# Optimization experiments

Hardware: AMD Instinct MI355X
Metric: run time of the kernel (lower is better)

Reference implementation:

```python
import jax, jax.numpy as jnp
import numpy as np

K = 3  # polynomial filter order

def gfgcn_layer(X, S, W, h, b):
    # X: [N, in], W: [in, out], h: [K], b: [out]
    X = X @ W
    X_out = h[0] * X
    Sx = X
    for k in range(1, K):
        Sx = S @ Sx                 # graph shift propagation
        X_out = X_out + h[k] * Sx   # scalar-weighted accumulate
    return X_out + b[None, :]


def setup_inputs() -> dict:
    key = jax.random.key(0)
    ks = jax.random.split(key, 12)
    N, in_dim, hid_dim, out_dim = 8192, 512, 128, 64
    # scale S so repeated propagation stays numerically tame
    S = jax.random.normal(ks[0], (N, N), dtype=jnp.float32) / jnp.sqrt(jnp.float32(N))
    X = jax.random.normal(ks[1], (N, in_dim), dtype=jnp.float32)
    def kaiming(k, shape):
        bound = np.sqrt(6.0 / shape[0])
        return jax.random.uniform(k, shape, jnp.float32, -bound, bound)
    W1 = kaiming(ks[2], (in_dim, hid_dim))
    W2 = kaiming(ks[3], (hid_dim, hid_dim))
    W3 = kaiming(ks[4], (hid_dim, out_dim))
    h1 = jnp.ones((K,), jnp.float32)
    h2 = jnp.ones((K,), jnp.float32)
    h3 = jnp.ones((K,), jnp.float32)
    b1 = jnp.zeros((hid_dim,), jnp.float32)
    b2 = jnp.zeros((hid_dim,), jnp.float32)
    b3 = jnp.zeros((out_dim,), jnp.float32)
    return {"S": S, "X": X, "W1": W1, "h1": h1, "b1": b1,
            "W2": W2, "h2": h2, "b2": b2, "W3": W3, "h3": h3, "b3": b3}


def reference(S, X, W1, h1, b1, W2, h2, b2, W3, h3, b3):
    # layer 1 + ReLU (dropout p=0 -> identity, batch_norm=False)
    X = jax.nn.relu(gfgcn_layer(X, S, W1, h1, b1))
    # layer 2 + ReLU
    X = jax.nn.relu(gfgcn_layer(X, S, W2, h2, b2))
    # last layer, last_act = Identity
    return gfgcn_layer(X, S, W3, h3, b3)
```

## Files before the change

### kernel.cpp

```cpp
#include <hip/hip_runtime.h>


typedef __attribute__((ext_vector_type(4))) float  f32x4;
typedef __attribute__((ext_vector_type(8))) __bf16 bf16x8;
typedef __attribute__((ext_vector_type(4))) __bf16 bf16x4;

__device__ __forceinline__ void gload_lds16(const __bf16* g, __bf16* l) {
    __builtin_amdgcn_global_load_lds(
        (const __attribute__((address_space(1))) void*)g,
        (__attribute__((address_space(3))) void*)l, 16, 0, 0);
}

__global__ void cvt_f32_bf16(const float4* __restrict__ in,
                             bf16x4* __restrict__ out, int n4) {
    int i  = blockIdx.x * blockDim.x + threadIdx.x;
    int st = gridDim.x * blockDim.x;
    for (; i < n4; i += st) {
        float4 v = in[i];
        bf16x4 o;
        o[0] = (__bf16)v.x; o[1] = (__bf16)v.y;
        o[2] = (__bf16)v.z; o[3] = (__bf16)v.w;
        out[i] = o;
    }
}

__global__ void cvt_transpose(const float* __restrict__ W,
                              __bf16* __restrict__ Wt, int Kd, int Md) {
    int i = blockIdx.x * blockDim.x + threadIdx.x;
    if (i < Kd * Md) {
        int k = i / Md, m = i % Md;
        Wt[(size_t)m * Kd + k] = (__bf16)W[i];
    }
}

template<int MF, int NF, int OUTMODE, int BF32>
__global__ __launch_bounds__(256)
void gemm_rd(const __bf16* __restrict__ A, const void* __restrict__ Bv,
             void* __restrict__ out, int K, int Kchunk, int Mtot, int Ntot)
{
    const int lane = threadIdx.x & 63;
    const int w    = threadIdx.x >> 6;
    const int l15  = lane & 15;
    const int quad = lane >> 4;

    const int m_base = blockIdx.x * (64 * MF) + w * (16 * MF);
    const int n_base = blockIdx.y * (16 * NF);
    const int kstart = blockIdx.z * Kchunk;

    const __bf16* Ap[MF];
    #pragma unroll
    for (int mf = 0; mf < MF; mf++)
        Ap[mf] = A + (size_t)(m_base + mf * 16 + l15) * K + kstart + quad * 8;

    const __bf16* Bp[NF];
    const float*  Bpf[NF];
    #pragma unroll
    for (int nf = 0; nf < NF; nf++) {
        const size_t roff = (size_t)(n_base + nf * 16 + l15) * K + kstart + quad * 8;
        if (BF32) Bpf[nf] = (const float*)Bv + roff;
        else      Bp[nf]  = (const __bf16*)Bv + roff;
    }

    f32x4 acc[MF][NF];
    #pragma unroll
    for (int mf = 0; mf < MF; mf++)
        #pragma unroll
        for (int nf = 0; nf < NF; nf++)
            acc[mf][nf] = (f32x4){0.f, 0.f, 0.f, 0.f};

    #pragma unroll 2
    for (int ks = 0; ks < Kchunk; ks += 32) {
        bf16x8 a[MF], b[NF];
        #pragma unroll
        for (int mf = 0; mf < MF; mf++) a[mf] = *(const bf16x8*)(Ap[mf] + ks);
        #pragma unroll
        for (int nf = 0; nf < NF; nf++) {
            if (BF32) {
                float4 f0 = *(const float4*)(Bpf[nf] + ks);
                float4 f1 = *(const float4*)(Bpf[nf] + ks + 4);
                bf16x8 tt;
                tt[0] = (__bf16)f0.x; tt[1] = (__bf16)f0.y;
                tt[2] = (__bf16)f0.z; tt[3] = (__bf16)f0.w;
                tt[4] = (__bf16)f1.x; tt[5] = (__bf16)f1.y;
                tt[6] = (__bf16)f1.z; tt[7] = (__bf16)f1.w;
                b[nf] = tt;
            } else {
                b[nf] = *(const bf16x8*)(Bp[nf] + ks);
            }
        }
        #pragma unroll
        for (int mf = 0; mf < MF; mf++)
            #pragma unroll
            for (int nf = 0; nf < NF; nf++)
                acc[mf][nf] = __builtin_amdgcn_mfma_f32_16x16x32_bf16(
                    a[mf], b[nf], acc[mf][nf], 0, 0, 0);
    }

    if (OUTMODE == 0) {
        float* P = (float*)out + (size_t)blockIdx.z * Mtot * Ntot;
        #pragma unroll
        for (int mf = 0; mf < MF; mf++) {
            const int rowb = m_base + mf * 16 + quad * 4;
            #pragma unroll
            for (int nf = 0; nf < NF; nf++) {
                const int col = n_base + nf * 16 + l15;
                *(f32x4*)(P + (size_t)col * Mtot + rowb) = acc[mf][nf];
            }
        }
    } else {
        __bf16* O = (__bf16*)out;
        #pragma unroll
        for (int mf = 0; mf < MF; mf++) {
            const int rowb = m_base + mf * 16 + quad * 4;
            #pragma unroll
            for (int nf = 0; nf < NF; nf++) {
                const int col = n_base + nf * 16 + l15;
                #pragma unroll
                for (int r = 0; r < 4; r++)
                    O[(size_t)(rowb + r) * Ntot + col] = (__bf16)acc[mf][nf][r];
            }
        }
    }
}

template<int NFW>
__global__ __launch_bounds__(256)
void sgemm_lds(const __bf16* __restrict__ A, const __bf16* __restrict__ Bt,
               float* __restrict__ P, int K, int Kchunk, int Mtot)
{
    constexpr int BN = 32 * NFW;
    __shared__ __bf16 Asm[3][64 * 32];
    __shared__ __bf16 Bsm[3][BN * 32];

    const int t    = threadIdx.x;
    const int lane = t & 63;
    const int w    = t >> 6;
    const int wm   = w >> 1;
    const int wn   = w & 1;
    const int l15  = lane & 15;
    const int quad = lane >> 4;

    const int m_block = blockIdx.x * 64;
    const int kstart  = blockIdx.z * Kchunk;
    const int nst     = Kchunk >> 5;

    const int rt  = t >> 2;
    const int qs  = (t & 3) ^ ((rt >> 1) & 3);
    const __bf16* gA  = A  + (size_t)(m_block + rt) * K + kstart + qs * 8;
    const __bf16* gB0 = Bt + (size_t)rt * K        + kstart + qs * 8;
    const __bf16* gB1 = Bt + (size_t)(64 + rt) * K + kstart + qs * 8;

    f32x4 acc[2][NFW];
    #pragma unroll
    for (int mf = 0; mf < 2; mf++)
        #pragma unroll
        for (int nf = 0; nf < NFW; nf++)
            acc[mf][nf] = (f32x4){0.f, 0.f, 0.f, 0.f};

    auto stage = [&](int buf, int st) {
        const int ks = st << 5;
        gload_lds16(gA  + ks, &Asm[buf][t * 8]);
        gload_lds16(gB0 + ks, &Bsm[buf][t * 8]);
        if (NFW == 4)
            gload_lds16(gB1 + ks, &Bsm[buf][2048 + t * 8]);
    };

    int aoff[2], boff[NFW];
    #pragma unroll
    for (int mf = 0; mf < 2; mf++) {
        const int ar = wm * 32 + mf * 16 + l15;
        aoff[mf] = ar * 32 + (quad ^ ((ar >> 1) & 3)) * 8;
    }
    #pragma unroll
    for (int nf = 0; nf < NFW; nf++) {
        const int br = wn * 16 * NFW + nf * 16 + l15;
        boff[nf] = br * 32 + (quad ^ ((br >> 1) & 3)) * 8;
    }

    stage(0, 0);
    if (nst > 1) stage(1, 1);
    if (nst > 2) stage(2, 2);

    for (int st = 0; st < nst; ++st) {
        const int rem   = nst - 1 - st;
        const int ahead = rem < 2 ? rem : 2;

        if (ahead == 2) {
            if (NFW == 4) asm volatile("s_waitcnt vmcnt(6)" ::: "memory");
            else          asm volatile("s_waitcnt vmcnt(4)" ::: "memory");
        } else if (ahead == 1) {
            if (NFW == 4) asm volatile("s_waitcnt vmcnt(3)" ::: "memory");
            else          asm volatile("s_waitcnt vmcnt(2)" ::: "memory");
        } else {
            asm volatile("s_waitcnt vmcnt(0)" ::: "memory");
        }
        __builtin_amdgcn_s_barrier();
        asm volatile("" ::: "memory");

        const int buf = st - (st / 3) * 3;
        bf16x8 a[2], b[NFW];
        #pragma unroll
        for (int mf = 0; mf < 2; mf++)
            a[mf] = *(const bf16x8*)&Asm[buf][aoff[mf]];
        #pragma unroll
        for (int nf = 0; nf < NFW; nf++)
            b[nf] = *(const bf16x8*)&Bsm[buf][boff[nf]];

        asm volatile("s_waitcnt lgkmcnt(0)" ::: "memory");
        __builtin_amdgcn_s_barrier();
        asm volatile("" ::: "memory");
        if (st + 3 < nst) stage(buf, st + 3);

        #pragma unroll
        for (int mf = 0; mf < 2; mf++)
            #pragma unroll
            for (int nf = 0; nf < NFW; nf++)
                acc[mf][nf] = __builtin_amdgcn_mfma_f32_16x16x32_bf16(
                    a[mf], b[nf], acc[mf][nf], 0, 0, 0);
    }

    float* Pz = P + (size_t)blockIdx.z * Mtot * BN;
    #pragma unroll
    for (int mf = 0; mf < 2; mf++) {
        const int rowb = m_block + wm * 32 + mf * 16 + quad * 4;
        #pragma unroll
        for (int nf = 0; nf < NFW; nf++) {
            const int col = wn * 16 * NFW + nf * 16 + l15;
            *(f32x4*)(Pz + (size_t)col * Mtot + rowb) = acc[mf][nf];
        }
    }
}

__global__ void reduce_partials(const float* __restrict__ P,
                                __bf16* __restrict__ Y, int total4,
                                int SP, int MN) {
    int i = blockIdx.x * blockDim.x + threadIdx.x;
    if (i >= total4) return;
    size_t base = (size_t)i * 4;
    float4 s = *(const float4*)(P + base);
    for (int sp = 1; sp < SP; sp++) {
        float4 v = *(const float4*)(P + (size_t)sp * MN + base);
        s.x += v.x; s.y += v.y; s.z += v.z; s.w += v.w;
    }
    bf16x4 o; o[0] = (__bf16)s.x; o[1] = (__bf16)s.y;
    o[2] = (__bf16)s.z; o[3] = (__bf16)s.w;
    *(bf16x4*)(Y + base) = o;
}

template<int RELU, int F32OUT>
__global__ void combine_out(const float* __restrict__ P,
                            const __bf16* __restrict__ Y0t,
                            const __bf16* __restrict__ Y1t,
                            const float* __restrict__ h,
                            const float* __restrict__ bias,
                            void* __restrict__ outp,
                            int F, int SP) {
    const int i = blockIdx.x * blockDim.x + threadIdx.x;
    const int total = F * 2048;
    if (i >= total) return;
    const int f  = i >> 11;
    const int n4 = i & 2047;
    const size_t base = (size_t)f * 8192 + (size_t)n4 * 4;
    const int MN = F * 8192;

    float4 s = *(const float4*)(P + base);
    for (int sp = 1; sp < SP; sp++) {
        float4 v = *(const float4*)(P + (size_t)sp * MN + base);
        s.x += v.x; s.y += v.y; s.z += v.z; s.w += v.w;
    }
    bf16x4 y0 = *(const bf16x4*)(Y0t + base);
    bf16x4 y1 = *(const bf16x4*)(Y1t + base);
    const float h0 = h[0], h1 = h[1], h2 = h[2], bb = bias[f];

    float v[4] = {s.x, s.y, s.z, s.w};
    #pragma unroll
    for (int r = 0; r < 4; r++) {
        float x = h0 * (float)y0[r] + h1 * (float)y1[r] + h2 * v[r] + bb;
        if (RELU) x = fmaxf(x, 0.0f);
        v[r] = x;
    }
    const int node = n4 * 4;
    if (F32OUT) {
        float* O = (float*)outp;
        #pragma unroll
        for (int r = 0; r < 4; r++) O[(size_t)(node + r) * F + f] = v[r];
    } else {
        __bf16* O = (__bf16*)outp;
        #pragma unroll
        for (int r = 0; r < 4; r++) O[(size_t)(node + r) * F + f] = (__bf16)v[r];
    }
}

extern "C" void kernel_launch(void* const* d_in, const int* in_sizes, int n_in,
                              void* d_out, int out_size, void* d_ws, size_t ws_size,
                              hipStream_t stream) {
    const float* S  = (const float*)d_in[0];
    const float* X  = (const float*)d_in[1];
    const float* W1 = (const float*)d_in[2];
    const float* h1 = (const float*)d_in[3];
    const float* b1 = (const float*)d_in[4];
    const float* W2 = (const float*)d_in[5];
    const float* h2 = (const float*)d_in[6];
    const float* b2 = (const float*)d_in[7];
    const float* W3 = (const float*)d_in[8];
    const float* h3 = (const float*)d_in[9];
    const float* b3 = (const float*)d_in[10];
    float* out = (float*)d_out;

    const int Nn = 8192, IN = 512, HID = 128, OUT = 64;

    char* ws = (char*)d_ws;
    size_t off = 0;
    auto carve = [&](size_t bytes) -> void* {
        void* p = ws + off;
        off += (bytes + 255) & ~(size_t)255;
        return p;
    };
    __bf16* Sb  = (__bf16*)carve((size_t)Nn * Nn  * 2);
    __bf16* W1t = (__bf16*)carve((size_t)IN  * HID * 2);
    __bf16* W2t = (__bf16*)carve((size_t)HID * HID * 2);
    __bf16* W3t = (__bf16*)carve((size_t)HID * OUT * 2);
    __bf16* Y0t = (__bf16*)carve((size_t)HID * Nn * 2);
    __bf16* Y1t = (__bf16*)carve((size_t)HID * Nn * 2);
    __bf16* Act = (__bf16*)carve((size_t)Nn * HID * 2);
    size_t  base = off;

    const size_t per_split = (size_t)HID * Nn * 4;
    int SP = 1;
    while (SP < 8 && base + (size_t)(SP * 2) * per_split <= ws_size) SP *= 2;
    float* P = (float*)carve((size_t)SP * per_split);
    const int KCH = Nn / SP;

    {
        int n4 = Nn * Nn / 4;
        cvt_f32_bf16<<<dim3(4096), dim3(256), 0, stream>>>(
            (const float4*)S, (bf16x4*)Sb, n4);
    }
    cvt_transpose<<<dim3((IN * HID + 255) / 256), dim3(256), 0, stream>>>(W1, W1t, IN, HID);
    cvt_transpose<<<dim3((HID * HID + 255) / 256), dim3(256), 0, stream>>>(W2, W2t, HID, HID);
    cvt_transpose<<<dim3((HID * OUT + 255) / 256), dim3(256), 0, stream>>>(W3, W3t, HID, OUT);

    auto sgemm = [&](const __bf16* Bt, int F) {
        if (F == 128)
            sgemm_lds<4><<<dim3(Nn / 64, 1, SP), dim3(256), 0, stream>>>(
                Sb, Bt, P, Nn, KCH, Nn);
        else
            sgemm_lds<2><<<dim3(Nn / 64, 1, SP), dim3(256), 0, stream>>>(
                Sb, Bt, P, Nn, KCH, Nn);
    };
    auto reduceY = [&](__bf16* Y, int F) {
        int t4 = F * 2048;
        reduce_partials<<<dim3((t4 + 255) / 256), dim3(256), 0, stream>>>(
            P, Y, t4, SP, F * Nn);
    };

    gemm_rd<2, 4, 1, 1><<<dim3(1, Nn / 64, 1), dim3(256), 0, stream>>>(
        W1t, X, Y0t, IN, IN, HID, Nn);
    sgemm(Y0t, HID);
    reduceY(Y1t, HID);
    sgemm(Y1t, HID);
    combine_out<1, 0><<<dim3(HID * 2048 / 256), dim3(256), 0, stream>>>(
        P, Y0t, Y1t, h1, b1, Act, HID, SP);

    gemm_rd<2, 4, 1, 0><<<dim3(1, Nn / 64, 1), dim3(256), 0, stream>>>(
        W2t, Act, Y0t, HID, HID, HID, Nn);
    sgemm(Y0t, HID);
    reduceY(Y1t, HID);
    sgemm(Y1t, HID);
    combine_out<1, 0><<<dim3(HID * 2048 / 256), dim3(256), 0, stream>>>(
        P, Y0t, Y1t, h2, b2, Act, HID, SP);

    gemm_rd<1, 4, 1, 0><<<dim3(1, Nn / 64, 1), dim3(256), 0, stream>>>(
        W3t, Act, Y0t, HID, HID, OUT, Nn);
    sgemm(Y0t, OUT);
    reduceY(Y1t, OUT);
    sgemm(Y1t, OUT);
    combine_out<0, 1><<<dim3(OUT * 2048 / 256), dim3(256), 0, stream>>>(
        P, Y0t, Y1t, h3, b3, out, OUT, SP);

    (void)in_sizes; (void)n_in; (void)out_size;
}
```

Baseline: 722.0 us.

## Pre-pack S into swizzled per-block tiles for contiguous LDS staging

Replaces the flat fp32-to-bf16 conversion of S with a packing kernel that writes S as bf16 in a tiled, pre-swizzled layout. Each (row-block, k-split) slab becomes contiguous, with 2048-element stages. The sgemm then loads A with a single contiguous 16-byte-per-thread stream instead of strided row reads, which is meant to improve coalescing and TLB behaviour across the six propagation GEMMs. The cost is a more complex pack kernel that goes through LDS and has two barriers per chunk, and that kernel may itself be slower than the plain conversion.

After: 695.5 us, median of 2. -3.7%, faster.

```diff
diff --git a/kernel.cpp b/kernel.cpp
--- a/kernel.cpp
+++ b/kernel.cpp
@@ -11,16 +11,46 @@
         (__attribute__((address_space(3))) void*)l, 16, 0, 0);
 }
 
-__global__ void cvt_f32_bf16(const float4* __restrict__ in,
-                             bf16x4* __restrict__ out, int n4) {
-    int i  = blockIdx.x * blockDim.x + threadIdx.x;
-    int st = gridDim.x * blockDim.x;
-    for (; i < n4; i += st) {
-        float4 v = in[i];
-        bf16x4 o;
-        o[0] = (__bf16)v.x; o[1] = (__bf16)v.y;
-        o[2] = (__bf16)v.z; o[3] = (__bf16)v.w;
-        out[i] = o;
+__global__ __launch_bounds__(256)
+void pack_S(const float* __restrict__ S, __bf16* __restrict__ Spk,
+            int KCH, int SP) {
+    __shared__ __bf16 L[8][1032];
+    const int t = threadIdx.x;
+    const int m = blockIdx.x, z = blockIdx.y;
+    __bf16* tile = Spk + ((size_t)m * SP + z) * ((size_t)64 * KCH);
+
+    const int rl    = t & 7;
+    const int cstep = t >> 3;
+    const int stl0  = t >> 5;
+    const int slot  = t & 31;
+    const int rs    = slot >> 2;
+    const int q     = slot & 3;
+
+    for (int r0 = 0; r0 < 64; r0 += 8) {
+        const int rg_st = r0 + rs;
+        const int qq    = q ^ ((rg_st >> 1) & 3);
+        for (int c1 = 0; c1 < KCH; c1 += 1024) {
+            const float* src = S + (size_t)(m * 64 + r0 + rl) * 8192
+                                 + (size_t)z * KCH + c1 + cstep * 32;
+            #pragma unroll
+            for (int j = 0; j < 4; j++) {
+                float4 f0 = *(const float4*)(src + j * 8);
+                float4 f1 = *(const float4*)(src + j * 8 + 4);
+                bf16x8 v;
+                v[0]=(__bf16)f0.x; v[1]=(__bf16)f0.y; v[2]=(__bf16)f0.z; v[3]=(__bf16)f0.w;
+                v[4]=(__bf16)f1.x; v[5]=(__bf16)f1.y; v[6]=(__bf16)f1.z; v[7]=(__bf16)f1.w;
+                *(bf16x8*)&L[rl][cstep * 32 + j * 8] = v;
+            }
+            __syncthreads();
+            #pragma unroll
+            for (int k2 = 0; k2 < 4; k2++) {
+                const int stl = stl0 + k2 * 8;
+                bf16x8 v = *(const bf16x8*)&L[rs][stl * 32 + qq * 8];
+                *(bf16x8*)(tile + (size_t)((c1 >> 5) + stl) * 2048
+                                + (size_t)(r0 * 4 + slot) * 8) = v;
+            }
+            __syncthreads();
+        }
     }
 }
 
@@ -125,8 +155,8 @@
 
 template<int NFW>
 __global__ __launch_bounds__(256)
-void sgemm_lds(const __bf16* __restrict__ A, const __bf16* __restrict__ Bt,
-               float* __restrict__ P, int K, int Kchunk, int Mtot)
+void sgemm_lds(const __bf16* __restrict__ Spk, const __bf16* __restrict__ Bt,
+               float* __restrict__ P, int Kb, int Kchunk, int Mtot)
 {
     constexpr int BN = 32 * NFW;
     __shared__ __bf16 Asm[3][64 * 32];
@@ -144,11 +174,13 @@
     const int kstart  = blockIdx.z * Kchunk;
     const int nst     = Kchunk >> 5;
 
+    const __bf16* gApk = Spk
+        + ((size_t)blockIdx.x * gridDim.z + blockIdx.z) * ((size_t)64 * Kchunk);
+
     const int rt  = t >> 2;
     const int qs  = (t & 3) ^ ((rt >> 1) & 3);
-    const __bf16* gA  = A  + (size_t)(m_block + rt) * K + kstart + qs * 8;
-    const __bf16* gB0 = Bt + (size_t)rt * K        + kstart + qs * 8;
-    const __bf16* gB1 = Bt + (size_t)(64 + rt) * K + kstart + qs * 8;
+    const __bf16* gB0 = Bt + (size_t)rt * Kb        + kstart + qs * 8;
+    const __bf16* gB1 = Bt + (size_t)(64 + rt) * Kb + kstart + qs * 8;
 
     f32x4 acc[2][NFW];
     #pragma unroll
@@ -158,8 +190,8 @@
             acc[mf][nf] = (f32x4){0.f, 0.f, 0.f, 0.f};
 
     auto stage = [&](int buf, int st) {
+        gload_lds16(gApk + (size_t)st * 2048 + t * 8, &Asm[buf][t * 8]);
         const int ks = st << 5;
-        gload_lds16(gA  + ks, &Asm[buf][t * 8]);
         gload_lds16(gB0 + ks, &Bsm[buf][t * 8]);
         if (NFW == 4)
             gload_lds16(gB1 + ks, &Bsm[buf][2048 + t * 8]);
@@ -316,7 +348,7 @@
         off += (bytes + 255) & ~(size_t)255;
         return p;
     };
-    __bf16* Sb  = (__bf16*)carve((size_t)Nn * Nn  * 2);
+    __bf16* Spk = (__bf16*)carve((size_t)Nn * Nn  * 2);
     __bf16* W1t = (__bf16*)carve((size_t)IN  * HID * 2);
     __bf16* W2t = (__bf16*)carve((size_t)HID * HID * 2);
     __bf16* W3t = (__bf16*)carve((size_t)HID * OUT * 2);
@@ -331,11 +363,7 @@
     float* P = (float*)carve((size_t)SP * per_split);
     const int KCH = Nn / SP;
 
-    {
-        int n4 = Nn * Nn / 4;
-        cvt_f32_bf16<<<dim3(4096), dim3(256), 0, stream>>>(
-            (const float4*)S, (bf16x4*)Sb, n4);
-    }
+    pack_S<<<dim3(Nn / 64, SP), dim3(256), 0, stream>>>(S, Spk, KCH, SP);
     cvt_transpose<<<dim3((IN * HID + 255) / 256), dim3(256), 0, stream>>>(W1, W1t, IN, HID);
     cvt_transpose<<<dim3((HID * HID + 255) / 256), dim3(256), 0, stream>>>(W2, W2t, HID, HID);
     cvt_transpose<<<dim3((HID * OUT + 255) / 256), dim3(256), 0, stream>>>(W3, W3t, HID, OUT);
@@ -343,10 +371,10 @@
     auto sgemm = [&](const __bf16* Bt, int F) {
         if (F == 128)
             sgemm_lds<4><<<dim3(Nn / 64, 1, SP), dim3(256), 0, stream>>>(
-                Sb, Bt, P, Nn, KCH, Nn);
+                Spk, Bt, P, Nn, KCH, Nn);
         else
             sgemm_lds<2><<<dim3(Nn / 64, 1, SP), dim3(256), 0, stream>>>(
-                Sb, Bt, P, Nn, KCH, Nn);
+                Spk, Bt, P, Nn, KCH, Nn);
     };
     auto reduceY = [&](__bf16* Y, int F) {
         int t4 = F * 2048;
```

## Replace split-K S-propagation GEMM with direct full-K kernel writing bf16

Applied to the files above, without the earlier changes.

Removes the split-K partitioning of the S@Y GEMMs and the fp32 partial buffers and reduction kernels. A new kernel uses 32-row tiles with K-steps of 64 over the full 8192 inner dimension and writes bf16 results directly. combine_out now reads a bf16 third term instead of summing fp32 partials. This drops the partial writes, the reduce pass and extra launches, but gives each block a long serial K loop with 256 blocks, and it rounds the last propagation term to bf16.

After: 929.2 us. 28.7% more time.

```diff
diff --git a/kernel.cpp b/kernel.cpp
--- a/kernel.cpp
+++ b/kernel.cpp
@@ -96,41 +96,31 @@
                     a[mf], b[nf], acc[mf][nf], 0, 0, 0);
     }
 
-    if (OUTMODE == 0) {
-        float* P = (float*)out + (size_t)blockIdx.z * Mtot * Ntot;
-        #pragma unroll
-        for (int mf = 0; mf < MF; mf++) {
-            const int rowb = m_base + mf * 16 + quad * 4;
+    __bf16* O = (__bf16*)out;
+    #pragma unroll
+    for (int mf = 0; mf < MF; mf++) {
+        const int rowb = m_base + mf * 16 + quad * 4;
+        #pragma unroll
+        for (int nf = 0; nf < NF; nf++) {
+            const int col = n_base + nf * 16 + l15;
             #pragma unroll
-            for (int nf = 0; nf < NF; nf++) {
-                const int col = n_base + nf * 16 + l15;
-                *(f32x4*)(P + (size_t)col * Mtot + rowb) = acc[mf][nf];
-            }
+            for (int r = 0; r < 4; r++)
+                O[(size_t)(rowb + r) * Ntot + col] = (__bf16)acc[mf][nf][r];
         }
-    } else {
-        __bf16* O = (__bf16*)out;
-        #pragma unroll
-        for (int mf = 0; mf < MF; mf++) {
-            const int rowb = m_base + mf * 16 + quad * 4;
-            #pragma unroll
-            for (int nf = 0; nf < NF; nf++) {
-                const int col = n_base + nf * 16 + l15;
-                #pragma unroll
-                for (int r = 0; r < 4; r++)
-                    O[(size_t)(rowb + r) * Ntot + col] = (__bf16)acc[mf][nf][r];
-            }
-        }
-    }
-}
-
-template<int NFW>
+    }
+    (void)Mtot;
+}
+
+template<int NF>
 __global__ __launch_bounds__(256)
-void sgemm_lds(const __bf16* __restrict__ A, const __bf16* __restrict__ Bt,
-               float* __restrict__ P, int K, int Kchunk, int Mtot)
+void sgemm_direct(const __bf16* __restrict__ A, const __bf16* __restrict__ Bt,
+                  __bf16* __restrict__ Z)
 {
-    constexpr int BN = 32 * NFW;
-    __shared__ __bf16 Asm[3][64 * 32];
-    __shared__ __bf16 Bsm[3][BN * 32];
+    constexpr int BN   = 32 * NF;
+    constexpr int LPS  = 1 + NF;
+    constexpr int DEPTH = 3;
+    __shared__ __bf16 Asm[DEPTH][32 * 64];
+    __shared__ __bf16 Bsm[DEPTH][BN * 64];
 
     const int t    = threadIdx.x;
     const int lane = t & 63;
@@ -140,142 +130,122 @@
     const int l15  = lane & 15;
     const int quad = lane >> 4;
 
-    const int m_block = blockIdx.x * 64;
-    const int kstart  = blockIdx.z * Kchunk;
-    const int nst     = Kchunk >> 5;
-
-    const int rt  = t >> 2;
-    const int qs  = (t & 3) ^ ((rt >> 1) & 3);
-    const __bf16* gA  = A  + (size_t)(m_block + rt) * K + kstart + qs * 8;
-    const __bf16* gB0 = Bt + (size_t)rt * K        + kstart + qs * 8;
-    const __bf16* gB1 = Bt + (size_t)(64 + rt) * K + kstart + qs * 8;
-
-    f32x4 acc[2][NFW];
-    #pragma unroll
-    for (int mf = 0; mf < 2; mf++)
-        #pragma unroll
-        for (int nf = 0; nf < NFW; nf++)
-            acc[mf][nf] = (f32x4){0.f, 0.f, 0.f, 0.f};
+    const int m_block = blockIdx.x * 32;
+    const int nst     = 8192 / 64;
+
+    const int ra = t >> 3, qa = t & 7;
+    const __bf16* gA = A + (size_t)(m_block + ra) * 8192 + (qa ^ (ra & 7)) * 8;
+    const __bf16* gBr[NF];
+    #pragma unroll
+    for (int j = 0; j < NF; j++) {
+        const int rb = j * 32 + (t >> 3), qb = t & 7;
+        gBr[j] = Bt + (size_t)rb * 8192 + (qb ^ (rb & 7)) * 8;
+    }
+
+    f32x4 acc[NF];
+    #pragma unroll
+    for (int nf = 0; nf < NF; nf++) acc[nf] = (f32x4){0.f, 0.f, 0.f, 0.f};
+
+    int aoff[2], boff[NF][2];
+    #pragma unroll
+    for (int h = 0; h < 2; h++) {
+        const int ar = wm * 16 + l15;
+        aoff[h] = ar * 64 + (((h * 4 + quad) ^ (ar & 7))) * 8;
+    }
+    #pragma unroll
+    for (int nf = 0; nf < NF; nf++)
+        #pragma unroll
+        for (int h = 0; h < 2; h++) {
+            const int br = wn * 16 * NF + nf * 16 + l15;
+            boff[nf][h] = br * 64 + (((h * 4 + quad) ^ (br & 7))) * 8;
+        }
 
     auto stage = [&](int buf, int st) {
-        const int ks = st << 5;
-        gload_lds16(gA  + ks, &Asm[buf][t * 8]);
-        gload_lds16(gB0 + ks, &Bsm[buf][t * 8]);
-        if (NFW == 4)
-            gload_lds16(gB1 + ks, &Bsm[buf][2048 + t * 8]);
+        const size_t ks = (size_t)st * 64;
+        gload_lds16(gA + ks, &Asm[buf][t * 8]);
+        #pragma unroll
+        for (int j = 0; j < NF; j++)
+            gload_lds16(gBr[j] + ks, &Bsm[buf][j * 2048 + t * 8]);
     };
 
-    int aoff[2], boff[NFW];
-    #pragma unroll
-    for (int mf = 0; mf < 2; mf++) {
-        const int ar = wm * 32 + mf * 16 + l15;
-        aoff[mf] = ar * 32 + (quad ^ ((ar >> 1) & 3)) * 8;
-    }
-    #pragma unroll
-    for (int nf = 0; nf < NFW; nf++) {
-        const int br = wn * 16 * NFW + nf * 16 + l15;
-        boff[nf] = br * 32 + (quad ^ ((br >> 1) & 3)) * 8;
-    }
-
-    stage(0, 0);
-    if (nst > 1) stage(1, 1);
-    if (nst > 2) stage(2, 2);
-
+    stage(0, 0); stage(1, 1); stage(2, 2);
+
+    int buf = 0;
     for (int st = 0; st < nst; ++st) {
         const int rem   = nst - 1 - st;
         const int ahead = rem < 2 ? rem : 2;
-
-        if (ahead == 2) {
-            if (NFW == 4) asm volatile("s_waitcnt vmcnt(6)" ::: "memory");
-            else          asm volatile("s_waitcnt vmcnt(4)" ::: "memory");
-        } else if (ahead == 1) {
-            if (NFW == 4) asm volatile("s_waitcnt vmcnt(3)" ::: "memory");
-            else          asm volatile("s_waitcnt vmcnt(2)" ::: "memory");
+        if (NF == 4) {
+            if      (ahead == 2) asm volatile("s_waitcnt vmcnt(10)" ::: "memory");
+            else if (ahead == 1) asm volatile("s_waitcnt vmcnt(5)"  ::: "memory");
+            else                 asm volatile("s_waitcnt vmcnt(0)"  ::: "memory");
         } else {
-            asm volatile("s_waitcnt vmcnt(0)" ::: "memory");
+            if      (ahead == 2) asm volatile("s_waitcnt vmcnt(6)" ::: "memory");
+            else if (ahead == 1) asm volatile("s_waitcnt vmcnt(3)" ::: "memory");
+            else                 asm volatile("s_waitcnt vmcnt(0)" ::: "memory");
         }
         __builtin_amdgcn_s_barrier();
         asm volatile("" ::: "memory");
 
-        const int buf = st - (st / 3) * 3;
-        bf16x8 a[2], b[NFW];
-        #pragma unroll
-        for (int mf = 0; mf < 2; mf++)
-            a[mf] = *(const bf16x8*)&Asm[buf][aoff[mf]];
-        #pragma unroll
-        for (int nf = 0; nf < NFW; nf++)
-            b[nf] = *(const bf16x8*)&Bsm[buf][boff[nf]];
+        bf16x8 a[2], b[NF][2];
+        #pragma unroll
+        for (int h = 0; h < 2; h++)
+            a[h] = *(const bf16x8*)&Asm[buf][aoff[h]];
+        #pragma unroll
+        for (int nf = 0; nf < NF; nf++)
+            #pragma unroll
+            for (int h = 0; h < 2; h++)
+                b[nf][h] = *(const bf16x8*)&Bsm[buf][boff[nf][h]];
 
         asm volatile("s_waitcnt lgkmcnt(0)" ::: "memory");
         __builtin_amdgcn_s_barrier();
         asm volatile("" ::: "memory");
-        if (st + 3 < nst) stage(buf, st + 3);
-
-        #pragma unroll
-        for (int mf = 0; mf < 2; mf++)
+        if (st + DEPTH < nst) stage(buf, st + DEPTH);
+
+        #pragma unroll
+        for (int h = 0; h < 2; h++)
             #pragma unroll
-            for (int nf = 0; nf < NFW; nf++)
-                acc[mf][nf] = __builtin_amdgcn_mfma_f32_16x16x32_bf16(
-                    a[mf], b[nf], acc[mf][nf], 0, 0, 0);
-    }
-
-    float* Pz = P + (size_t)blockIdx.z * Mtot * BN;
-    #pragma unroll
-    for (int mf = 0; mf < 2; mf++) {
-        const int rowb = m_block + wm * 32 + mf * 16 + quad * 4;
-        #pragma unroll
-        for (int nf = 0; nf < NFW; nf++) {
-            const int col = wn * 16 * NFW + nf * 16 + l15;
-            *(f32x4*)(Pz + (size_t)col * Mtot + rowb) = acc[mf][nf];
-        }
-    }
-}
-
-__global__ void reduce_partials(const float* __restrict__ P,
-                                __bf16* __restrict__ Y, int total4,
-                                int SP, int MN) {
-    int i = blockIdx.x * blockDim.x + threadIdx.x;
-    if (i >= total4) return;
-    size_t base = (size_t)i * 4;
-    float4 s = *(const float4*)(P + base);
-    for (int sp = 1; sp < SP; sp++) {
-        float4 v = *(const float4*)(P + (size_t)sp * MN + base);
-        s.x += v.x; s.y += v.y; s.z += v.z; s.w += v.w;
-    }
-    bf16x4 o; o[0] = (__bf16)s.x; o[1] = (__bf16)s.y;
-    o[2] = (__bf16)s.z; o[3] = (__bf16)s.w;
-    *(bf16x4*)(Y + base) = o;
+            for (int nf = 0; nf < NF; nf++)
+                acc[nf] = __builtin_amdgcn_mfma_f32_16x16x32_bf16(
+                    a[h], b[nf][h], acc[nf], 0, 0, 0);
+
+        buf = (buf + 1 == DEPTH) ? 0 : buf + 1;
+        (void)LPS;
+    }
+
+    const int row0 = m_block + wm * 16 + quad * 4;
+    #pragma unroll
+    for (int nf = 0; nf < NF; nf++) {
+        const int col = wn * 16 * NF + nf * 16 + l15;
+        bf16x4 o;
+        o[0] = (__bf16)acc[nf][0]; o[1] = (__bf16)acc[nf][1];
+        o[2] = (__bf16)acc[nf][2]; o[3] = (__bf16)acc[nf][3];
+        *(bf16x4*)(Z + (size_t)col * 8192 + row0) = o;
+    }
 }
 
 template<int RELU, int F32OUT>
-__global__ void combine_out(const float* __restrict__ P,
-                            const __bf16* __restrict__ Y0t,
+__global__ void combine_out(const __bf16* __restrict__ Y0t,
                             const __bf16* __restrict__ Y1t,
+                            const __bf16* __restrict__ Zt,
                             const float* __restrict__ h,
                             const float* __restrict__ bias,
-                            void* __restrict__ outp,
-                            int F, int SP) {
+                            void* __restrict__ outp, int F) {
     const int i = blockIdx.x * blockDim.x + threadIdx.x;
     const int total = F * 2048;
     if (i >= total) return;
     const int f  = i >> 11;
     const int n4 = i & 2047;
     const size_t base = (size_t)f * 8192 + (size_t)n4 * 4;
-    const int MN = F * 8192;
-
-    float4 s = *(const float4*)(P + base);
-    for (int sp = 1; sp < SP; sp++) {
-        float4 v = *(const float4*)(P + (size_t)sp * MN + base);
-        s.x += v.x; s.y += v.y; s.z += v.z; s.w += v.w;
-    }
+
     bf16x4 y0 = *(const bf16x4*)(Y0t + base);
     bf16x4 y1 = *(const bf16x4*)(Y1t + base);
+    bf16x4 z  = *(const bf16x4*)(Zt  + base);
     const float h0 = h[0], h1 = h[1], h2 = h[2], bb = bias[f];
 
-    float v[4] = {s.x, s.y, s.z, s.w};
+    float v[4];
     #pragma unroll
     for (int r = 0; r < 4; r++) {
-        float x = h0 * (float)y0[r] + h1 * (float)y1[r] + h2 * v[r] + bb;
+        float x = h0 * (float)y0[r] + h1 * (float)y1[r] + h2 * (float)z[r] + bb;
         if (RELU) x = fmaxf(x, 0.0f);
         v[r] = x;
     }
@@ -322,61 +292,37 @@
     __bf16* W3t = (__bf16*)carve((size_t)HID * OUT * 2);
     __bf16* Y0t = (__bf16*)carve((size_t)HID * Nn * 2);
     __bf16* Y1t = (__bf16*)carve((size_t)HID * Nn * 2);
+    __bf16* Zt  = (__bf16*)carve((size_t)HID * Nn * 2);
     __bf16* Act = (__bf16*)carve((size_t)Nn * HID * 2);
-    size_t  base = off;
-
-    const size_t per_split = (size_t)HID * Nn * 4;
-    int SP = 1;
-    while (SP < 8 && base + (size_t)(SP * 2) * per_split <= ws_size) SP *= 2;
-    float* P = (float*)carve((size_t)SP * per_split);
-    const int KCH = Nn / SP;
-
-    {
-        int n4 = Nn * Nn / 4;
-        cvt_f32_bf16<<<dim3(4096), dim3(256), 0, stream>>>(
-            (const float4*)S, (bf16x4*)Sb, n4);
-    }
+
+    cvt_f32_bf16<<<dim3(4096), dim3(256), 0, stream>>>(
+        (const float4*)S, (bf16x4*)Sb, Nn * Nn / 4);
     cvt_transpose<<<dim3((IN * HID + 255) / 256), dim3(256), 0, stream>>>(W1, W1t, IN, HID);
     cvt_transpose<<<dim3((HID * HID + 255) / 256), dim3(256), 0, stream>>>(W2, W2t, HID, HID);
     cvt_transpose<<<dim3((HID * OUT + 255) / 256), dim3(256), 0, stream>>>(W3, W3t, HID, OUT);
 
-    auto sgemm = [&](const __bf16* Bt, int F) {
-        if (F == 128)
-            sgemm_lds<4><<<dim3(Nn / 64, 1, SP), dim3(256), 0, stream>>>(
-                Sb, Bt, P, Nn, KCH, Nn);
-        else
-            sgemm_lds<2><<<dim3(Nn / 64, 1, SP), dim3(256), 0, stream>>>(
-                Sb, Bt, P, Nn, KCH, Nn);
-    };
-    auto reduceY = [&](__bf16* Y, int F) {
-        int t4 = F * 2048;
-        reduce_partials<<<dim3((t4 + 255) / 256), dim3(256), 0, stream>>>(
-            P, Y, t4, SP, F * Nn);
-    };
+    const dim3 sgrid(Nn / 32, 1, 1);
 
     gemm_rd<2, 4, 1, 1><<<dim3(1, Nn / 64, 1), dim3(256), 0, stream>>>(
         W1t, X, Y0t, IN, IN, HID, Nn);
-    sgemm(Y0t, HID);
-    reduceY(Y1t, HID);
-    sgemm(Y1t, HID);
+    sgemm_direct<4><<<sgrid, dim3(256), 0, stream>>>(Sb, Y0t, Y1t);
+    sgemm_direct<4><<<sgrid, dim3(256), 0, stream>>>(Sb, Y1t, Zt);
     combine_out<1, 0><<<dim3(HID * 2048 / 256), dim3(256), 0, stream>>>(
-        P, Y0t, Y1t, h1, b1, Act, HID, SP);
+        Y0t, Y1t, Zt, h1, b1, Act, HID);
 
     gemm_rd<2, 4, 1, 0><<<dim3(1, Nn / 64, 1), dim3(256), 0, stream>>>(
         W2t, Act, Y0t, HID, HID, HID, Nn);
-    sgemm(Y0t, HID);
-    reduceY(Y1t, HID);
-    sgemm(Y1t, HID);
+    sgemm_direct<4><<<sgrid, dim3(256), 0, stream>>>(Sb, Y0t, Y1t);
+    sgemm_direct<4><<<sgrid, dim3(256), 0, stream>>>(Sb, Y1t, Zt);
     combine_out<1, 0><<<dim3(HID * 2048 / 256), dim3(256), 0, stream>>>(
-        P, Y0t, Y1t, h2, b2, Act, HID, SP);
+        Y0t, Y1t, Zt, h2, b2, Act, HID);
 
     gemm_rd<1, 4, 1, 0><<<dim3(1, Nn / 64, 1), dim3(256), 0, stream>>>(
         W3t, Act, Y0t, HID, HID, OUT, Nn);
-    sgemm(Y0t, OUT);
-    reduceY(Y1t, OUT);
-    sgemm(Y1t, OUT);
+    sgemm_direct<2><<<sgrid, dim3(256), 0, stream>>>(Sb, Y0t, Y1t);
+    sgemm_direct<2><<<sgrid, dim3(256), 0, stream>>>(Sb, Y1t, Zt);
     combine_out<0, 1><<<dim3(OUT * 2048 / 256), dim3(256), 0, stream>>>(
-        P, Y0t, Y1t, h3, b3, out, OUT, SP);
-
-    (void)in_sizes; (void)n_in; (void)out_size;
-}
+        Y0t, Y1t, Zt, h3, b3, out, OUT);
+
+    (void)in_sizes; (void)n_in; (void)out_size; (void)ws_size;
+}
```

## Replace direct global-to-LDS loads with register-staged double buffering and blob partial layout

Applied to the files above, without the earlier changes.

The S-propagation GEMM stops using global_load_lds with triple buffering. It now loads tiles into registers two steps ahead and writes them to a double-buffered LDS after the barrier. Partial sums are stored in the MFMA fragment order as contiguous float4 blobs, and the reduce and combine kernels decode that order back to rows and columns. This is meant to make the partial stores fully coalesced and change how load latency is hidden, at the cost of higher register pressure, hardcoded N=8192 strides, and scattered writes in the reduce step.

Result: faster. 707.9 us (-2.0%).

```diff
diff --git a/kernel.cpp b/kernel.cpp
--- a/kernel.cpp
+++ b/kernel.cpp
@@ -4,12 +4,6 @@
 typedef __attribute__((ext_vector_type(4))) float  f32x4;
 typedef __attribute__((ext_vector_type(8))) __bf16 bf16x8;
 typedef __attribute__((ext_vector_type(4))) __bf16 bf16x4;
-
-__device__ __forceinline__ void gload_lds16(const __bf16* g, __bf16* l) {
-    __builtin_amdgcn_global_load_lds(
-        (const __attribute__((address_space(1))) void*)g,
-        (__attribute__((address_space(3))) void*)l, 16, 0, 0);
-}
 
 __global__ void cvt_f32_bf16(const float4* __restrict__ in,
                              bf16x4* __restrict__ out, int n4) {
@@ -96,41 +90,29 @@
                     a[mf], b[nf], acc[mf][nf], 0, 0, 0);
     }
 
-    if (OUTMODE == 0) {
-        float* P = (float*)out + (size_t)blockIdx.z * Mtot * Ntot;
-        #pragma unroll
-        for (int mf = 0; mf < MF; mf++) {
-            const int rowb = m_base + mf * 16 + quad * 4;
+    __bf16* O = (__bf16*)out;
+    #pragma unroll
+    for (int mf = 0; mf < MF; mf++) {
+        const int rowb = m_base + mf * 16 + quad * 4;
+        #pragma unroll
+        for (int nf = 0; nf < NF; nf++) {
+            const int col = n_base + nf * 16 + l15;
             #pragma unroll
-            for (int nf = 0; nf < NF; nf++) {
-                const int col = n_base + nf * 16 + l15;
-                *(f32x4*)(P + (size_t)col * Mtot + rowb) = acc[mf][nf];
-            }
+            for (int r = 0; r < 4; r++)
+                O[(size_t)(rowb + r) * Ntot + col] = (__bf16)acc[mf][nf][r];
         }
-    } else {
-        __bf16* O = (__bf16*)out;
-        #pragma unroll
-        for (int mf = 0; mf < MF; mf++) {
-            const int rowb = m_base + mf * 16 + quad * 4;
-            #pragma unroll
-            for (int nf = 0; nf < NF; nf++) {
-                const int col = n_base + nf * 16 + l15;
-                #pragma unroll
-                for (int r = 0; r < 4; r++)
-                    O[(size_t)(rowb + r) * Ntot + col] = (__bf16)acc[mf][nf][r];
-            }
-        }
-    }
+    }
+    (void)Mtot; (void)OUTMODE;
 }
 
 template<int NFW>
 __global__ __launch_bounds__(256)
-void sgemm_lds(const __bf16* __restrict__ A, const __bf16* __restrict__ Bt,
-               float* __restrict__ P, int K, int Kchunk, int Mtot)
+void sgemm_rs(const __bf16* __restrict__ A, const __bf16* __restrict__ Bt,
+              float* __restrict__ P, int Kchunk)
 {
     constexpr int BN = 32 * NFW;
-    __shared__ __bf16 Asm[3][64 * 32];
-    __shared__ __bf16 Bsm[3][BN * 32];
+    __shared__ __bf16 Asm[2][64 * 32];
+    __shared__ __bf16 Bsm[2][BN * 32];
 
     const int t    = threadIdx.x;
     const int lane = t & 63;
@@ -144,26 +126,15 @@
     const int kstart  = blockIdx.z * Kchunk;
     const int nst     = Kchunk >> 5;
 
-    const int rt  = t >> 2;
-    const int qs  = (t & 3) ^ ((rt >> 1) & 3);
-    const __bf16* gA  = A  + (size_t)(m_block + rt) * K + kstart + qs * 8;
-    const __bf16* gB0 = Bt + (size_t)rt * K        + kstart + qs * 8;
-    const __bf16* gB1 = Bt + (size_t)(64 + rt) * K + kstart + qs * 8;
-
-    f32x4 acc[2][NFW];
-    #pragma unroll
-    for (int mf = 0; mf < 2; mf++)
-        #pragma unroll
-        for (int nf = 0; nf < NFW; nf++)
-            acc[mf][nf] = (f32x4){0.f, 0.f, 0.f, 0.f};
-
-    auto stage = [&](int buf, int st) {
-        const int ks = st << 5;
-        gload_lds16(gA  + ks, &Asm[buf][t * 8]);
-        gload_lds16(gB0 + ks, &Bsm[buf][t * 8]);
-        if (NFW == 4)
-            gload_lds16(gB1 + ks, &Bsm[buf][2048 + t * 8]);
-    };
+    const int rt = t >> 2, q = t & 3;
+    const __bf16* gA  = A  + (size_t)(m_block + rt) * 8192 + kstart + q * 8;
+    const __bf16* gB0 = Bt + (size_t)rt * 8192        + kstart + q * 8;
+    const __bf16* gB1 = Bt + (size_t)(64 + rt) * 8192 + kstart + q * 8;
+
+    const int swz  = (q ^ ((rt >> 1) & 3)) * 8;
+    const int awr  = rt * 32 + swz;
+    const int bwr0 = rt * 32 + swz;
+    const int bwr1 = 2048 + rt * 32 + swz;
 
     int aoff[2], boff[NFW];
     #pragma unroll
@@ -177,117 +148,145 @@
         boff[nf] = br * 32 + (quad ^ ((br >> 1) & 3)) * 8;
     }
 
-    stage(0, 0);
-    if (nst > 1) stage(1, 1);
-    if (nst > 2) stage(2, 2);
-
-    for (int st = 0; st < nst; ++st) {
-        const int rem   = nst - 1 - st;
-        const int ahead = rem < 2 ? rem : 2;
-
-        if (ahead == 2) {
-            if (NFW == 4) asm volatile("s_waitcnt vmcnt(6)" ::: "memory");
-            else          asm volatile("s_waitcnt vmcnt(4)" ::: "memory");
-        } else if (ahead == 1) {
-            if (NFW == 4) asm volatile("s_waitcnt vmcnt(3)" ::: "memory");
-            else          asm volatile("s_waitcnt vmcnt(2)" ::: "memory");
-        } else {
-            asm volatile("s_waitcnt vmcnt(0)" ::: "memory");
-        }
-        __builtin_amdgcn_s_barrier();
-        asm volatile("" ::: "memory");
-
-        const int buf = st - (st / 3) * 3;
-        bf16x8 a[2], b[NFW];
-        #pragma unroll
-        for (int mf = 0; mf < 2; mf++)
-            a[mf] = *(const bf16x8*)&Asm[buf][aoff[mf]];
+    f32x4 acc[2][NFW];
+    #pragma unroll
+    for (int mf = 0; mf < 2; mf++)
         #pragma unroll
         for (int nf = 0; nf < NFW; nf++)
-            b[nf] = *(const bf16x8*)&Bsm[buf][boff[nf]];
-
+            acc[mf][nf] = (f32x4){0.f, 0.f, 0.f, 0.f};
+
+    auto ld_set = [&](bf16x8& ra, bf16x8 (&rb)[2], int st) {
+        const size_t ks = (size_t)st << 5;
+        ra    = *(const bf16x8*)(gA  + ks);
+        rb[0] = *(const bf16x8*)(gB0 + ks);
+        if constexpr (NFW == 4) rb[1] = *(const bf16x8*)(gB1 + ks);
+    };
+    auto dsw = [&](int buf, const bf16x8& ra, const bf16x8 (&rb)[2]) {
+        *(bf16x8*)&Asm[buf][awr]  = ra;
+        *(bf16x8*)&Bsm[buf][bwr0] = rb[0];
+        if constexpr (NFW == 4) *(bf16x8*)&Bsm[buf][bwr1] = rb[1];
+    };
+    auto iter = [&](int st, bf16x8& ra_i, bf16x8 (&rb_i)[2],
+                    bf16x8& ra_w, bf16x8 (&rb_w)[2]) {
         asm volatile("s_waitcnt lgkmcnt(0)" ::: "memory");
         __builtin_amdgcn_s_barrier();
         asm volatile("" ::: "memory");
-        if (st + 3 < nst) stage(buf, st + 3);
-
-        #pragma unroll
-        for (int mf = 0; mf < 2; mf++)
-            #pragma unroll
-            for (int nf = 0; nf < NFW; nf++)
-                acc[mf][nf] = __builtin_amdgcn_mfma_f32_16x16x32_bf16(
-                    a[mf], b[nf], acc[mf][nf], 0, 0, 0);
-    }
-
-    float* Pz = P + (size_t)blockIdx.z * Mtot * BN;
-    #pragma unroll
-    for (int mf = 0; mf < 2; mf++) {
-        const int rowb = m_block + wm * 32 + mf * 16 + quad * 4;
+        if (st + 2 < nst) ld_set(ra_i, rb_i, st + 2);
+
+        const int buf = st & 1;
+        bf16x8 a0 = *(const bf16x8*)&Asm[buf][aoff[0]];
+        bf16x8 a1 = *(const bf16x8*)&Asm[buf][aoff[1]];
+        bf16x8 bb[NFW];
+        #pragma unroll
+        for (int nf = 0; nf < NFW; nf++)
+            bb[nf] = *(const bf16x8*)&Bsm[buf][boff[nf]];
+
+        asm volatile("s_waitcnt lgkmcnt(0)" ::: "memory");
+        __builtin_amdgcn_s_barrier();
+        asm volatile("" ::: "memory");
+        if (st + 1 < nst) dsw((st + 1) & 1, ra_w, rb_w);
+
+        #pragma unroll
+        for (int nf = 0; nf < NFW; nf++)
+            acc[0][nf] = __builtin_amdgcn_mfma_f32_16x16x32_bf16(
+                a0, bb[nf], acc[0][nf], 0, 0, 0);
+        #pragma unroll
+        for (int nf = 0; nf < NFW; nf++)
+            acc[1][nf] = __builtin_amdgcn_mfma_f32_16x16x32_bf16(
+                a1, bb[nf], acc[1][nf], 0, 0, 0);
+    };
+
+    bf16x8 raS0, raS1;
+    bf16x8 rbS0[2], rbS1[2];
+    ld_set(raS0, rbS0, 0);
+    ld_set(raS1, rbS1, 1);
+    dsw(0, raS0, rbS0);
+
+    for (int st = 0; st < nst; st += 2) {
+        iter(st,     raS0, rbS0, raS1, rbS1);
+        iter(st + 1, raS1, rbS1, raS0, rbS0);
+    }
+
+    float* Pz = P + (size_t)blockIdx.z * (size_t)8192 * BN;
+    #pragma unroll
+    for (int mf = 0; mf < 2; mf++)
         #pragma unroll
         for (int nf = 0; nf < NFW; nf++) {
-            const int col = wn * 16 * NFW + nf * 16 + l15;
-            *(f32x4*)(Pz + (size_t)col * Mtot + rowb) = acc[mf][nf];
+            const size_t q4 = ((((size_t)blockIdx.x * 4 + w) * 2 + mf) * NFW + nf) * 64 + lane;
+            *(f32x4*)(Pz + q4 * 4) = acc[mf][nf];
         }
-    }
-}
-
-__global__ void reduce_partials(const float* __restrict__ P,
-                                __bf16* __restrict__ Y, int total4,
-                                int SP, int MN) {
-    int i = blockIdx.x * blockDim.x + threadIdx.x;
+}
+
+template<int NFW>
+__global__ void reduce_blob(const float* __restrict__ P,
+                            __bf16* __restrict__ Y, int total4, int SP) {
+    const int i = blockIdx.x * blockDim.x + threadIdx.x;
     if (i >= total4) return;
-    size_t base = (size_t)i * 4;
-    float4 s = *(const float4*)(P + base);
+    constexpr int LB = (NFW == 4) ? 2 : 1;
+    const int lane = i & 63;
+    const int nf   = (i >> 6) & (NFW - 1);
+    const int mf   = (i >> (6 + LB)) & 1;
+    const int w    = (i >> (7 + LB)) & 3;
+    const int mblk = i >> (9 + LB);
+    const int col  = (w & 1) * 16 * NFW + nf * 16 + (lane & 15);
+    const int row  = mblk * 64 + (w >> 1) * 32 + mf * 16 + (lane >> 4) * 4;
+    const size_t MN = (size_t)total4 * 4;
+
+    float4 s = *(const float4*)(P + (size_t)i * 4);
     for (int sp = 1; sp < SP; sp++) {
-        float4 v = *(const float4*)(P + (size_t)sp * MN + base);
+        float4 v = *(const float4*)(P + (size_t)sp * MN + (size_t)i * 4);
         s.x += v.x; s.y += v.y; s.z += v.z; s.w += v.w;
     }
     bf16x4 o; o[0] = (__bf16)s.x; o[1] = (__bf16)s.y;
     o[2] = (__bf16)s.z; o[3] = (__bf16)s.w;
-    *(bf16x4*)(Y + base) = o;
-}
-
-template<int RELU, int F32OUT>
-__global__ void combine_out(const float* __restrict__ P,
-                            const __bf16* __restrict__ Y0t,
-                            const __bf16* __restrict__ Y1t,
-                            const float* __restrict__ h,
-                            const float* __restrict__ bias,
-                            void* __restrict__ outp,
-                            int F, int SP) {
+    *(bf16x4*)(Y + (size_t)col * 8192 + row) = o;
+}
+
+template<int NFW, int RELU, int F32OUT>
+__global__ void combine_blob(const float* __restrict__ P,
+                             const __bf16* __restrict__ Y0t,
+                             const __bf16* __restrict__ Y1t,
+                             const float* __restrict__ h,
+                             const float* __restrict__ bias,
+                             void* __restrict__ outp, int total4, int SP) {
     const int i = blockIdx.x * blockDim.x + threadIdx.x;
-    const int total = F * 2048;
-    if (i >= total) return;
-    const int f  = i >> 11;
-    const int n4 = i & 2047;
-    const size_t base = (size_t)f * 8192 + (size_t)n4 * 4;
-    const int MN = F * 8192;
-
-    float4 s = *(const float4*)(P + base);
+    if (i >= total4) return;
+    constexpr int F  = 32 * NFW;
+    constexpr int LB = (NFW == 4) ? 2 : 1;
+    const int lane = i & 63;
+    const int nf   = (i >> 6) & (NFW - 1);
+    const int mf   = (i >> (6 + LB)) & 1;
+    const int w    = (i >> (7 + LB)) & 3;
+    const int mblk = i >> (9 + LB);
+    const int col  = (w & 1) * 16 * NFW + nf * 16 + (lane & 15);
+    const int row  = mblk * 64 + (w >> 1) * 32 + mf * 16 + (lane >> 4) * 4;
+    const size_t MN = (size_t)total4 * 4;
+
+    float4 s = *(const float4*)(P + (size_t)i * 4);
     for (int sp = 1; sp < SP; sp++) {
-        float4 v = *(const float4*)(P + (size_t)sp * MN + base);
+        float4 v = *(const float4*)(P + (size_t)sp * MN + (size_t)i * 4);
         s.x += v.x; s.y += v.y; s.z += v.z; s.w += v.w;
     }
-    bf16x4 y0 = *(const bf16x4*)(Y0t + base);
-    bf16x4 y1 = *(const bf16x4*)(Y1t + base);
-    const float h0 = h[0], h1 = h[1], h2 = h[2], bb = bias[f];
-
-    float v[4] = {s.x, s.y, s.z, s.w};
+    bf16x4 y0 = *(const bf16x4*)(Y0t + (size_t)col * 8192 + row);
+    bf16x4 y1 = *(const bf16x4*)(Y1t + (size_t)col * 8192 + row);
+    const float h0 = h[0], h1 = h[1], h2 = h[2], bb = bias[col];
+
+    float sv[4] = {s.x, s.y, s.z, s.w};
+    float v[4];
     #pragma unroll
     for (int r = 0; r < 4; r++) {
-        float x = h0 * (float)y0[r] + h1 * (float)y1[r] + h2 * v[r] + bb;
+        float x = h0 * (float)y0[r] + h1 * (float)y1[r] + h2 * sv[r] + bb;
         if (RELU) x = fmaxf(x, 0.0f);
         v[r] = x;
     }
-    const int node = n4 * 4;
     if (F32OUT) {
         float* O = (float*)outp;
         #pragma unroll
-        for (int r = 0; r < 4; r++) O[(size_t)(node + r) * F + f] = v[r];
+        for (int r = 0; r < 4; r++) O[(size_t)(row + r) * F + col] = v[r];
     } else {
         __bf16* O = (__bf16*)outp;
         #pragma unroll
-        for (int r = 0; r < 4; r++) O[(size_t)(node + r) * F + f] = (__bf16)v[r];
+        for (int r = 0; r < 4; r++) O[(size_t)(row + r) * F + col] = (__bf16)v[r];
     }
 }
 
@@ -331,27 +330,24 @@
     float* P = (float*)carve((size_t)SP * per_split);
     const int KCH = Nn / SP;
 
-    {
-        int n4 = Nn * Nn / 4;
-        cvt_f32_bf16<<<dim3(4096), dim3(256), 0, stream>>>(
-            (const float4*)S, (bf16x4*)Sb, n4);
-    }
+    cvt_f32_bf16<<<dim3(4096), dim3(256), 0, stream>>>(
+        (const float4*)S, (bf16x4*)Sb, Nn * Nn / 4);
     cvt_transpose<<<dim3((IN * HID + 255) / 256), dim3(256), 0, stream>>>(W1, W1t, IN, HID);
     cvt_transpose<<<dim3((HID * HID + 255) / 256), dim3(256), 0, stream>>>(W2, W2t, HID, HID);
     cvt_transpose<<<dim3((HID * OUT + 255) / 256), dim3(256), 0, stream>>>(W3, W3t, HID, OUT);
 
     auto sgemm = [&](const __bf16* Bt, int F) {
         if (F == 128)
-            sgemm_lds<4><<<dim3(Nn / 64, 1, SP), dim3(256), 0, stream>>>(
-                Sb, Bt, P, Nn, KCH, Nn);
+            sgemm_rs<4><<<dim3(Nn / 64, 1, SP), dim3(256), 0, stream>>>(Sb, Bt, P, KCH);
         else
-            sgemm_lds<2><<<dim3(Nn / 64, 1, SP), dim3(256), 0, stream>>>(
-                Sb, Bt, P, Nn, KCH, Nn);
+            sgemm_rs<2><<<dim3(Nn / 64, 1, SP), dim3(256), 0, stream>>>(Sb, Bt, P, KCH);
     };
     auto reduceY = [&](__bf16* Y, int F) {
-        int t4 = F * 2048;
-        reduce_partials<<<dim3((t4 + 255) / 256), dim3(256), 0, stream>>>(
-            P, Y, t4, SP, F * Nn);
+        const int t4 = 2048 * F;
+        if (F == 128)
+            reduce_blob<4><<<dim3((t4 + 255) / 256), dim3(256), 0, stream>>>(P, Y, t4, SP);
+        else
+            reduce_blob<2><<<dim3((t4 + 255) / 256), dim3(256), 0, stream>>>(P, Y, t4, SP);
     };
 
     gemm_rd<2, 4, 1, 1><<<dim3(1, Nn / 64, 1), dim3(256), 0, stream>>>(
@@ -359,24 +355,24 @@
     sgemm(Y0t, HID);
     reduceY(Y1t, HID);
     sgemm(Y1t, HID);
-    combine_out<1, 0><<<dim3(HID * 2048 / 256), dim3(256), 0, stream>>>(
-        P, Y0t, Y1t, h1, b1, Act, HID, SP);
+    combine_blob<4, 1, 0><<<dim3(2048 * HID / 256), dim3(256), 0, stream>>>(
+        P, Y0t, Y1t, h1, b1, Act, 2048 * HID, SP);
 
     gemm_rd<2, 4, 1, 0><<<dim3(1, Nn / 64, 1), dim3(256), 0, stream>>>(
         W2t, Act, Y0t, HID, HID, HID, Nn);
     sgemm(Y0t, HID);
     reduceY(Y1t, HID);
     sgemm(Y1t, HID);
-    combine_out<1, 0><<<dim3(HID * 2048 / 256), dim3(256), 0, stream>>>(
-        P, Y0t, Y1t, h2, b2, Act, HID, SP);
+    combine_blob<4, 1, 0><<<dim3(2048 * HID / 256), dim3(256), 0, stream>>>(
+        P, Y0t, Y1t, h2, b2, Act, 2048 * HID, SP);
 
     gemm_rd<1, 4, 1, 0><<<dim3(1, Nn / 64, 1), dim3(256), 0, stream>>>(
         W3t, Act, Y0t, HID, HID, OUT, Nn);
     sgemm(Y0t, OUT);
     reduceY(Y1t, OUT);
     sgemm(Y1t, OUT);
-    combine_out<0, 1><<<dim3(OUT * 2048 / 256), dim3(256), 0, stream>>>(
-        P, Y0t, Y1t, h3, b3, out, OUT, SP);
+    combine_blob<2, 0, 1><<<dim3(2048 * OUT / 256), dim3(256), 0, stream>>>(
+        P, Y0t, Y1t, h3, b3, out, 2048 * OUT, SP);
 
     (void)in_sizes; (void)n_in; (void)out_size;
 }
```
